# Optimization experiments

Hardware: AMD Instinct MI355X
Metric: run time of the kernel (lower is better)

Reference implementation:

```python
import jax, jax.numpy as jnp
import numpy as np

T, B, IN_DIM, H, N_RESETS = 4096, 256, 128, 8, 32


def setup_inputs() -> dict:
    key = jax.random.key(0)
    ks = jax.random.split(key, 8)
    s = 1.0 / np.sqrt(H)  # PyTorch LSTM/Linear init scale
    return {
        "x": jax.random.normal(ks[0], (T, B, IN_DIM), jnp.float32),
        "reset_idx": jnp.sort(jax.random.randint(ks[1], (N_RESETS,), 0, T)),
        "W_ih": jax.random.uniform(ks[2], (4 * H, IN_DIM), jnp.float32, -s, s),
        "W_hh": jax.random.uniform(ks[3], (4 * H, H), jnp.float32, -s, s),
        "b_ih": jax.random.uniform(ks[4], (4 * H,), jnp.float32, -s, s),
        "b_hh": jax.random.uniform(ks[5], (4 * H,), jnp.float32, -s, s),
        "W_proj": jax.random.uniform(ks[6], (1, H), jnp.float32, -s, s),
        "b_proj": jax.random.uniform(ks[7], (1,), jnp.float32, -s, s),
    }


def reference(x, reset_idx, W_ih, W_hh, b_ih, b_hh, W_proj, b_proj):
    # x: [T, B, in_dim] (batch_first=False).  reset_idx: timesteps where the
    # LSTM hidden/cell state is reset to zero before processing that step.
    Tn = x.shape[0]
    Bn = x.shape[1]
    Hn = W_hh.shape[1]
    reset_mask = jnp.zeros((Tn,), dtype=bool).at[reset_idx].set(True)

    # Precompute the input contribution to the gates for all timesteps at once
    # (this is the bulk of the FLOPs; only the small HxH recurrence stays in scan).
    x_gates = jnp.einsum("tbi,gi->tbg", x, W_ih) + b_ih + b_hh  # [T, B, 4H]

    def step(carry, inp):
        h, c = carry  # [B, H] each
        xg, rt = inp  # [B, 4H], scalar bool
        h = jnp.where(rt, jnp.zeros_like(h), h)
        c = jnp.where(rt, jnp.zeros_like(c), c)
        gates = xg + h @ W_hh.T  # [B, 4H]
        i, f, g, o = jnp.split(gates, 4, axis=-1)  # PyTorch gate order i,f,g,o
        c = jax.nn.sigmoid(f) * c + jax.nn.sigmoid(i) * jnp.tanh(g)
        h = jax.nn.sigmoid(o) * jnp.tanh(c)
        return (h, c), h

    h0 = jnp.zeros((Bn, Hn), x.dtype)
    c0 = jnp.zeros((Bn, Hn), x.dtype)
    (_, _), rnn_out = jax.lax.scan(step, (h0, c0), (x_gates, reset_mask))

    value = rnn_out @ W_proj.T + b_proj  # [T, B, 1]
    return (value, rnn_out)
```

## Files before the change

kernel.cpp:

```cpp
#include <hip/hip_runtime.h>
#include <cstdint>

#define TT 4096
#define BB 256
#define ID 128

typedef float f32x4 __attribute__((ext_vector_type(4)));
typedef short s16x8 __attribute__((ext_vector_type(8)));

__device__ __forceinline__ float rcp_fast(float x) { return __builtin_amdgcn_rcpf(x); }
__device__ __forceinline__ float sigm(float x) { return rcp_fast(1.0f + __expf(-x)); }
__device__ __forceinline__ float tanh_fast(float x) {
  float e = __expf(2.0f * x);
  return 1.0f - 2.0f * rcp_fast(e + 1.0f);
}

union U16B { uint32_t u[4]; s16x8 v; };

__device__ __forceinline__ void split8(const float4 a, const float4 b,
                                       s16x8& hi, s16x8& lo) {
  uint32_t a0 = __float_as_uint(a.x), a1 = __float_as_uint(a.y);
  uint32_t a2 = __float_as_uint(a.z), a3 = __float_as_uint(a.w);
  uint32_t b0 = __float_as_uint(b.x), b1 = __float_as_uint(b.y);
  uint32_t b2 = __float_as_uint(b.z), b3 = __float_as_uint(b.w);
  U16B h;
  h.u[0] = (a0 >> 16) | (a1 & 0xffff0000u);
  h.u[1] = (a2 >> 16) | (a3 & 0xffff0000u);
  h.u[2] = (b0 >> 16) | (b1 & 0xffff0000u);
  h.u[3] = (b2 >> 16) | (b3 & 0xffff0000u);
  hi = h.v;
  float r0 = a.x - __uint_as_float(a0 & 0xffff0000u);
  float r1 = a.y - __uint_as_float(a1 & 0xffff0000u);
  float r2 = a.z - __uint_as_float(a2 & 0xffff0000u);
  float r3 = a.w - __uint_as_float(a3 & 0xffff0000u);
  float r4 = b.x - __uint_as_float(b0 & 0xffff0000u);
  float r5 = b.y - __uint_as_float(b1 & 0xffff0000u);
  float r6 = b.z - __uint_as_float(b2 & 0xffff0000u);
  float r7 = b.w - __uint_as_float(b3 & 0xffff0000u);
  U16B l;
  l.u[0] = (__float_as_uint(r0) >> 16) | (__float_as_uint(r1) & 0xffff0000u);
  l.u[1] = (__float_as_uint(r2) >> 16) | (__float_as_uint(r3) & 0xffff0000u);
  l.u[2] = (__float_as_uint(r4) >> 16) | (__float_as_uint(r5) & 0xffff0000u);
  l.u[3] = (__float_as_uint(r6) >> 16) | (__float_as_uint(r7) & 0xffff0000u);
  lo = l.v;
}

__global__ __launch_bounds__(64) void prep_kernel(
    const float* __restrict__ W_ih, const float* __restrict__ b_ih,
    const float* __restrict__ b_hh,
    s16x8* __restrict__ whi, s16x8* __restrict__ wlo, float* __restrict__ bo)
{
  const int lane = threadIdx.x;
  const int kq   = (lane >> 4) * 2;
  const float4* __restrict__ w4 = reinterpret_cast<const float4*>(W_ih);
#pragma unroll
  for (int kc = 0; kc < 4; ++kc) {
#pragma unroll
    for (int nf = 0; nf < 2; ++nf) {
      int m  = nf * 16 + (lane & 15);
      int gp = (m & 3) * 8 + (m >> 2);
      int q0 = kc * 8 + kq;
      float4 wa = w4[gp * 32 + q0];
      float4 wb = w4[gp * 32 + q0 + 1];
      s16x8 hi, lo;
      split8(wa, wb, hi, lo);
      whi[(kc * 2 + nf) * 64 + lane] = hi;
      wlo[(kc * 2 + nf) * 64 + lane] = lo;
    }
  }
  if (lane < 32) {
    int gp = (lane & 3) * 8 + (lane >> 2);
    bo[lane] = b_ih[gp] + b_hh[gp];
  }
}

__global__ __launch_bounds__(256) void gates_kernel(
    const float* __restrict__ x,
    const s16x8* __restrict__ whi, const s16x8* __restrict__ wlo,
    const float* __restrict__ bo, float* __restrict__ xg)
{
  __shared__ float4 xt[64 * 32];
  const int tid = threadIdx.x;
  const size_t row0 = (size_t)blockIdx.x * 64;

  const float4* __restrict__ src = reinterpret_cast<const float4*>(x) + row0 * 32;
#pragma unroll
  for (int it = 0; it < 8; ++it) {
    int idx = it * 256 + tid;
    int r = idx >> 5, q = idx & 31;
    xt[r * 32 + (q ^ (r & 31))] = src[idx];
  }

  const int lane = tid & 63;
  const int wv   = tid >> 6;
  const int rloc = wv * 16 + (lane & 15);
  const int kq   = (lane >> 4) * 2;

  s16x8 Bh[4][2], Bl[4][2];
#pragma unroll
  for (int kc = 0; kc < 4; ++kc) {
#pragma unroll
    for (int nf = 0; nf < 2; ++nf) {
      Bh[kc][nf] = whi[(kc * 2 + nf) * 64 + lane];
      Bl[kc][nf] = wlo[(kc * 2 + nf) * 64 + lane];
    }
  }
  const float bo0 = bo[lane & 15];
  const float bo1 = bo[16 + (lane & 15)];

  __syncthreads();

  f32x4 acc[2] = {{0.f, 0.f, 0.f, 0.f}, {0.f, 0.f, 0.f, 0.f}};
#pragma unroll
  for (int kc = 0; kc < 4; ++kc) {
    int q0 = kc * 8 + kq;
    float4 xa = xt[rloc * 32 + (q0 ^ (rloc & 31))];
    float4 xb = xt[rloc * 32 + ((q0 + 1) ^ (rloc & 31))];
    s16x8 Ah, Al;
    split8(xa, xb, Ah, Al);
#pragma unroll
    for (int nf = 0; nf < 2; ++nf) {
      acc[nf] = __builtin_amdgcn_mfma_f32_16x16x32_bf16(Ah, Bh[kc][nf], acc[nf], 0, 0, 0);
      acc[nf] = __builtin_amdgcn_mfma_f32_16x16x32_bf16(Ah, Bl[kc][nf], acc[nf], 0, 0, 0);
      acc[nf] = __builtin_amdgcn_mfma_f32_16x16x32_bf16(Al, Bh[kc][nf], acc[nf], 0, 0, 0);
    }
  }

#pragma unroll
  for (int nf = 0; nf < 2; ++nf) {
    int m = nf * 16 + (lane & 15);
    float b = nf ? bo1 : bo0;
    size_t rowg = row0 + wv * 16 + (lane >> 4) * 4;
#pragma unroll
    for (int reg = 0; reg < 4; ++reg) {
      xg[(rowg + reg) * 32 + m] = acc[nf][reg] + b;
    }
  }
}

__global__ __launch_bounds__(64) void rnn_kernel(
    const float* __restrict__ xg, const int* __restrict__ reset_idx,
    const float* __restrict__ W_hh, const float* __restrict__ W_proj,
    const float* __restrict__ b_proj, float* __restrict__ out)
{
  const int seg  = blockIdx.x;
  const int lane = threadIdx.x;
  const int j    = lane & 7;
  const int b    = blockIdx.y * 8 + (lane >> 3);

  const int start = (seg == 0)  ? 0  : reset_idx[seg - 1];
  const int end   = (seg == 32) ? TT : reset_idx[seg];
  if (start >= end) return;

  float wi[8], wf[8], wg_[8], wo[8];
#pragma unroll
  for (int k = 0; k < 8; ++k) {
    wi[k]  = W_hh[(0  + j) * 8 + k];
    wf[k]  = W_hh[(8  + j) * 8 + k];
    wg_[k] = W_hh[(16 + j) * 8 + k];
    wo[k]  = W_hh[(24 + j) * 8 + k];
  }
  const float bp = b_proj[0];
  float wp[8];
#pragma unroll
  for (int k = 0; k < 8; ++k) wp[k] = W_proj[k];

  float h[8];
#pragma unroll
  for (int k = 0; k < 8; ++k) h[k] = 0.f;
  float c = 0.f;

  float* __restrict__ vout = out;
  float* __restrict__ hout = out + (size_t)TT * BB;

  const float4* __restrict__ xg4 = reinterpret_cast<const float4*>(xg);
  const size_t lbase = (size_t)b * 8 + j;

  float4 bufA[8], bufB[8];

#define LOADC(buf, tc) do {                                                  \
  _Pragma("unroll")                                                          \
  for (int s = 0; s < 8; ++s) {                                              \
    int tt = (tc) + s; tt = tt < TT ? tt : TT - 1;   \
    (buf)[s] = xg4[(size_t)tt * 2048 + lbase];                               \
  }                                                                          \
} while (0)

#define STEP8(buf, tc) do {                                                  \
  _Pragma("unroll")                                                          \
  for (int s = 0; s < 8; ++s) {                                              \
    int t = (tc) + s;                                                        \
    if (t < end) {                                  \
      float gi = (buf)[s].x, gf = (buf)[s].y;                                \
      float gg = (buf)[s].z, go = (buf)[s].w;                                \
      float gi1 = 0.f, gf1 = 0.f, gg1 = 0.f, go1 = 0.f;                      \
      _Pragma("unroll")                                                      \
      for (int k = 0; k < 8; k += 2) {                                       \
        gi += wi[k]  * h[k];  gi1 += wi[k+1]  * h[k+1];                      \
        gf += wf[k]  * h[k];  gf1 += wf[k+1]  * h[k+1];                      \
        gg += wg_[k] * h[k];  gg1 += wg_[k+1] * h[k+1];                      \
        go += wo[k]  * h[k];  go1 += wo[k+1]  * h[k+1];                      \
      }                                                                      \
      gi += gi1; gf += gf1; gg += gg1; go += go1;                            \
      float si = sigm(gi), sf = sigm(gf), sg = tanh_fast(gg), so = sigm(go); \
      c = sf * c + si * sg;                                                  \
      float hj = so * tanh_fast(c);                                          \
      hout[((size_t)t * BB + b) * 8 + j] = hj;                               \
      _Pragma("unroll")                                                      \
      for (int k = 0; k < 8; ++k) h[k] = __shfl(hj, k, 8);                   \
      float sv = bp;                                                         \
      _Pragma("unroll")                                                      \
      for (int k = 0; k < 8; ++k) sv += wp[k] * h[k];                        \
      if (j == 0) vout[(size_t)t * BB + b] = sv;                             \
    }                                                                        \
  }                                                                          \
} while (0)

  LOADC(bufA, start);
  LOADC(bufB, start + 8);
  for (int tc = start; tc < end; tc += 16) {
    STEP8(bufA, tc);
    LOADC(bufA, tc + 16);
    STEP8(bufB, tc + 8);
    LOADC(bufB, tc + 24);
  }
#undef LOADC
#undef STEP8
}

extern "C" void kernel_launch(void* const* d_in, const int* in_sizes, int n_in,
                              void* d_out, int out_size, void* d_ws, size_t ws_size,
                              hipStream_t stream) {
  const float* x      = (const float*)d_in[0];
  const int*   ridx   = (const int*)  d_in[1];
  const float* W_ih   = (const float*)d_in[2];
  const float* W_hh   = (const float*)d_in[3];
  const float* b_ih   = (const float*)d_in[4];
  const float* b_hh   = (const float*)d_in[5];
  const float* W_proj = (const float*)d_in[6];
  const float* b_proj = (const float*)d_in[7];
  float* out = (float*)d_out;

  float* xg  = (float*)d_ws;
  char*  aux = (char*)d_ws + (size_t)134217728;
  s16x8* whi = (s16x8*)aux;
  s16x8* wlo = whi + 512;
  float* bo  = (float*)(wlo + 512);

  prep_kernel<<<1, 64, 0, stream>>>(W_ih, b_ih, b_hh, whi, wlo, bo);
  gates_kernel<<<(TT * BB) / 64, 256, 0, stream>>>(x, whi, wlo, bo, xg);
  rnn_kernel<<<dim3(33, 32), 64, 0, stream>>>(xg, ridx, W_hh, W_proj, b_proj, out);
}
```

Baseline: 253.8 us.

## Double-buffer input tiles with async global-to-LDS loads in gates kernel

The gates kernel now handles 8 consecutive 64-row tiles per block instead of one. It stages each next tile into a second LDS buffer with global_load_lds while the current tile runs through the MFMA split-bf16 GEMM, and uses explicit vmcnt waits instead of a block barrier. The aim is to hide global load latency behind compute and to amortize the per-block weight-register loads over more tiles. In exchange there are 8x fewer blocks and double the LDS per block, and correctness depends on each wave touching only its own rows and on the hand-tuned vmcnt counts.

```diff
diff --git a/kernel.cpp b/kernel.cpp
--- a/kernel.cpp
+++ b/kernel.cpp
@@ -4,6 +4,7 @@
 #define TT 4096
 #define BB 256
 #define ID 128
+#define NT 8
 
 typedef float f32x4 __attribute__((ext_vector_type(4)));
 typedef short s16x8 __attribute__((ext_vector_type(8)));
@@ -79,23 +80,16 @@
     const s16x8* __restrict__ whi, const s16x8* __restrict__ wlo,
     const float* __restrict__ bo, float* __restrict__ xg)
 {
-  __shared__ float4 xt[64 * 32];
-  const int tid = threadIdx.x;
-  const size_t row0 = (size_t)blockIdx.x * 64;
-
-  const float4* __restrict__ src = reinterpret_cast<const float4*>(x) + row0 * 32;
-#pragma unroll
-  for (int it = 0; it < 8; ++it) {
-    int idx = it * 256 + tid;
-    int r = idx >> 5, q = idx & 31;
-    xt[r * 32 + (q ^ (r & 31))] = src[idx];
-  }
-
+  __shared__ float4 xt[2][64 * 32];
+  const int tid  = threadIdx.x;
   const int lane = tid & 63;
   const int wv   = tid >> 6;
   const int rloc = wv * 16 + (lane & 15);
   const int kq   = (lane >> 4) * 2;
 
+  const float4* __restrict__ x4 = reinterpret_cast<const float4*>(x);
+  const size_t tile0 = (size_t)blockIdx.x * NT;
+
   s16x8 Bh[4][2], Bl[4][2];
 #pragma unroll
   for (int kc = 0; kc < 4; ++kc) {
@@ -108,34 +102,62 @@
   const float bo0 = bo[lane & 15];
   const float bo1 = bo[16 + (lane & 15)];
 
-  __syncthreads();
-
-  f32x4 acc[2] = {{0.f, 0.f, 0.f, 0.f}, {0.f, 0.f, 0.f, 0.f}};
-#pragma unroll
-  for (int kc = 0; kc < 4; ++kc) {
-    int q0 = kc * 8 + kq;
-    float4 xa = xt[rloc * 32 + (q0 ^ (rloc & 31))];
-    float4 xb = xt[rloc * 32 + ((q0 + 1) ^ (rloc & 31))];
-    s16x8 Ah, Al;
-    split8(xa, xb, Ah, Al);
+#define STAGE(buf, tile) do {                                                  \
+    const float4* tsrc_ = x4 + (size_t)(tile) * 2048;                          \
+    _Pragma("unroll")                                                          \
+    for (int it_ = 0; it_ < 8; ++it_) {                                        \
+      int s_ = (wv * 8 + it_) * 64 + lane;                                     \
+      int r_ = s_ >> 5;                                                        \
+      int q_ = (s_ & 31) ^ (r_ & 31);                                          \
+      __builtin_amdgcn_global_load_lds(                                        \
+          (const __attribute__((address_space(1))) void*)(tsrc_ + r_ * 32 + q_), \
+          (__attribute__((address_space(3))) void*)(&xt[(buf)][(wv * 8 + it_) * 64]), \
+          16, 0, 0);                                                           \
+    }                                                                          \
+  } while (0)
+
+  STAGE(0, tile0);
+
+#pragma unroll 1
+  for (int t = 0; t < NT; ++t) {
+    const int cur = t & 1;
+    if (t + 1 < NT) STAGE(cur ^ 1, tile0 + t + 1);
+
+    if (t == 0 || t + 1 >= NT) {
+      asm volatile("s_waitcnt vmcnt(8)" ::: "memory");
+    } else {
+      asm volatile("s_waitcnt vmcnt(16)" ::: "memory");
+    }
+
+    f32x4 acc[2] = {{0.f, 0.f, 0.f, 0.f}, {0.f, 0.f, 0.f, 0.f}};
+#pragma unroll
+    for (int kc = 0; kc < 4; ++kc) {
+      int q0 = kc * 8 + kq;
+      float4 xa = xt[cur][rloc * 32 + (q0 ^ (rloc & 31))];
+      float4 xb = xt[cur][rloc * 32 + ((q0 + 1) ^ (rloc & 31))];
+      s16x8 Ah, Al;
+      split8(xa, xb, Ah, Al);
+#pragma unroll
+      for (int nf = 0; nf < 2; ++nf) {
+        acc[nf] = __builtin_amdgcn_mfma_f32_16x16x32_bf16(Ah, Bh[kc][nf], acc[nf], 0, 0, 0);
+        acc[nf] = __builtin_amdgcn_mfma_f32_16x16x32_bf16(Ah, Bl[kc][nf], acc[nf], 0, 0, 0);
+        acc[nf] = __builtin_amdgcn_mfma_f32_16x16x32_bf16(Al, Bh[kc][nf], acc[nf], 0, 0, 0);
+      }
+    }
+
+    const size_t row0 = (tile0 + t) * 64;
 #pragma unroll
     for (int nf = 0; nf < 2; ++nf) {
-      acc[nf] = __builtin_amdgcn_mfma_f32_16x16x32_bf16(Ah, Bh[kc][nf], acc[nf], 0, 0, 0);
-      acc[nf] = __builtin_amdgcn_mfma_f32_16x16x32_bf16(Ah, Bl[kc][nf], acc[nf], 0, 0, 0);
-      acc[nf] = __builtin_amdgcn_mfma_f32_16x16x32_bf16(Al, Bh[kc][nf], acc[nf], 0, 0, 0);
-    }
-  }
-
-#pragma unroll
-  for (int nf = 0; nf < 2; ++nf) {
-    int m = nf * 16 + (lane & 15);
-    float b = nf ? bo1 : bo0;
-    size_t rowg = row0 + wv * 16 + (lane >> 4) * 4;
-#pragma unroll
-    for (int reg = 0; reg < 4; ++reg) {
-      xg[(rowg + reg) * 32 + m] = acc[nf][reg] + b;
-    }
-  }
+      int m = nf * 16 + (lane & 15);
+      float bb = nf ? bo1 : bo0;
+      size_t rowg = row0 + wv * 16 + (lane >> 4) * 4;
+#pragma unroll
+      for (int reg = 0; reg < 4; ++reg) {
+        xg[(rowg + reg) * 32 + m] = acc[nf][reg] + bb;
+      }
+    }
+  }
+#undef STAGE
 }
 
 __global__ __launch_bounds__(64) void rnn_kernel(
@@ -248,6 +270,6 @@
   float* bo  = (float*)(wlo + 512);
 
   prep_kernel<<<1, 64, 0, stream>>>(W_ih, b_ih, b_hh, whi, wlo, bo);
-  gates_kernel<<<(TT * BB) / 64, 256, 0, stream>>>(x, whi, wlo, bo, xg);
+  gates_kernel<<<(TT * BB) / (64 * NT), 256, 0, stream>>>(x, whi, wlo, bo, xg);
   rnn_kernel<<<dim3(33, 32), 64, 0, stream>>>(xg, ridx, W_hh, W_proj, b_proj, out);
 }
```

Result: no change. 258.8 us (+2.0%).
